# Performance work log

Hardware: AMD Instinct MI355X
Metric: run time of the kernel (lower is better)

## Reference

```python
import jax, jax.numpy as jnp
import numpy as np
from jax import lax

GRID_SIZE = 3


def setup_inputs() -> dict:
    key = jax.random.key(0)
    k1, k2, k3 = jax.random.split(key, 3)
    B, Cin, Cout, H, W, KH, KW, G = 32, 64, 64, 64, 64, 3, 3, GRID_SIZE
    x = jax.random.normal(k1, (B, Cin, H, W), dtype=jnp.float32)
    scale_base = jax.random.normal(k2, (Cout, Cin, KH, KW), dtype=jnp.float32) * 0.1
    scale_spline = jnp.ones((Cout, Cin, KH, KW), dtype=jnp.float32)
    coeff = jax.random.normal(k3, (2, Cout, Cin, KH, KW, G), dtype=jnp.float32) * 0.02
    bias = jnp.zeros((Cout,), dtype=jnp.float32)
    return {"x": x, "scale_base": scale_base, "scale_spline": scale_spline, "coeff": coeff, "bias": bias}


def _conv(x, w, padding=1):
    return lax.conv_general_dilated(
        x, w, window_strides=(1, 1), padding=((padding, padding), (padding, padding)),
        dimension_numbers=("NCHW", "OIHW", "NCHW"))


def reference(x, scale_base, scale_spline, coeff, bias):
    B, Cin, H, W = x.shape
    Cout, _, KH, KW = scale_base.shape
    G = coeff.shape[-1]
    # Fourier feature expansion: cos(k*x), sin(k*x) for k = 1..G
    ks = jnp.arange(1, G + 1, dtype=x.dtype)
    xk = x[:, :, None] * ks[None, None, :, None, None]          # (B, Cin, G, H, W)
    feats = jnp.concatenate([jnp.cos(xk), jnp.sin(xk)], axis=2)  # (B, Cin, 2G, H, W)
    feats = feats.reshape(B, Cin * 2 * G, H, W)
    # Spline weights: coeff (2, Cout, Cin, KH, KW, G) scaled per-tap -> (Cout, Cin*2G, KH, KW)
    w = coeff * scale_spline[None, :, :, :, :, None]
    w = jnp.transpose(w, (1, 2, 0, 5, 3, 4)).reshape(Cout, Cin * 2 * G, KH, KW)
    # Base branch: SiLU(x) convolved with scale_base
    base = jax.nn.silu(x)
    out = _conv(base, scale_base) + _conv(feats, w)
    out = out + bias[None, :, None, None]
    return out
```

## Files before the change

kernel.cpp:

```cpp
#include <hip/hip_runtime.h>

typedef __attribute__((ext_vector_type(8))) short bf16x8;
typedef __attribute__((ext_vector_type(4))) float f32x4;

#define FROW   4224
#define FBUF   42240
#define BGRP   36864
#define LDS_TOT (2 * FBUF + 2 * BGRP)

static __device__ __forceinline__ unsigned short f2bf(float f) {
  union { float f; unsigned u; } v; v.f = f;
  unsigned r = v.u + 0x7fffu + ((v.u >> 16) & 1u);
  return (unsigned short)(r >> 16);
}

static __device__ __forceinline__ void gload16(const void* g, void* l) {
  __builtin_amdgcn_global_load_lds(
      (const __attribute__((address_space(1))) void*)g,
      (__attribute__((address_space(3))) void*)l, 16, 0, 0);
}

__global__ void pack_w_k(const float* __restrict__ sb, const float* __restrict__ ss,
                         const float* __restrict__ cf, unsigned short* __restrict__ wpk) {
  int idx = blockIdx.x * 256 + threadIdx.x;
  if (idx >= 126 * 64 * 32) return;
  int e = idx & 7;
  int q = (idx >> 3) & 3;
  int co = (idx >> 5) & 63;
  int rest = idx >> 11;
  int tap = rest % 9;
  int c2 = rest / 9;
  int c = c2 >> 1, half = c2 & 1;
  int ci = half * 32 + q * 8 + e;
  int kh = tap / 3, kw = tap % 3;
  int wi = ((co * 64 + ci) * 3 + kh) * 3 + kw;
  float v;
  if (c == 0) {
    v = sb[wi];
  } else {
    int s = (c - 1) / 3, g = (c - 1) % 3;
    v = cf[(s * 36864 + wi) * 3 + g] * ss[wi];
  }
  wpk[((c2 * 9 + tap) * 64 + co) * 32 + ((q ^ ((co >> 1) & 3)) << 3) + e] = f2bf(v);
}

__global__ void feats_k(const float* __restrict__ x, unsigned short* __restrict__ fg) {
  __shared__ __align__(16) unsigned short lds[64 * 456];
  const int b = blockIdx.x, h = blockIdx.y;
  const int tid = threadIdx.x;
  const int w = tid & 63, cig = tid >> 6;
  const int key = ((w + 1) >> 1) & 3;
  const int base = w * 456;
#pragma unroll
  for (int i = 0; i < 16; ++i) {
    int ci = cig * 16 + i;
    float v = x[(((size_t)b * 64 + ci) * 64 + h) * 64 + w];
    float sg = 1.0f / (1.0f + __expf(-v));
    float f0 = v * sg;
    float s1, c1;
    __sincosf(v, &s1, &c1);
    float c2v = c1 * c1 - s1 * s1, s2v = 2.0f * s1 * c1;
    float c3v = c1 * c2v - s1 * s2v, s3v = s1 * c2v + c1 * s2v;
    int q = ci >> 3;
    int half = q >> 2, qq = q & 3;
    int sl = (half * 4 + (qq ^ key)) * 8 + (ci & 7);
    lds[base + 0 * 64 + sl] = f2bf(f0);
    lds[base + 1 * 64 + sl] = f2bf(c1);
    lds[base + 2 * 64 + sl] = f2bf(c2v);
    lds[base + 3 * 64 + sl] = f2bf(c3v);
    lds[base + 4 * 64 + sl] = f2bf(s1);
    lds[base + 5 * 64 + sl] = f2bf(s2v);
    lds[base + 6 * 64 + sl] = f2bf(s3v);
  }
  __syncthreads();
#pragma unroll
  for (int k = 0; k < 14; ++k) {
    int u = tid + k * 256;
    int qs = u & 3;
    int ww = (u >> 2) & 63;
    int c2i = u >> 8;
    int cc = c2i >> 1, half = c2i & 1;
    uint4 v = *(const uint4*)&lds[ww * 456 + cc * 64 + (half * 4 + qs) * 8];
    unsigned short* dst = fg + ((size_t)(c2i * 32 + b) * 64 + h) * 2048 + (ww * 4 + qs) * 8;
    *(uint4*)dst = v;
  }
}

__global__ __launch_bounds__(512, 2) void gemm_k(
    const unsigned short* __restrict__ fg, const unsigned short* __restrict__ wpk,
    const float* __restrict__ bias, float* __restrict__ out) {
  extern __shared__ __align__(16) char smem[];
  const int b = blockIdx.x;
  const int h0 = blockIdx.y * 8;
  const int tid = threadIdx.x;
  const int lane = tid & 63;
  const int wid = tid >> 6;
  const int l15 = lane & 15;
  const int lg = lane >> 4;
  const char* fgB = (const char*)fg;
  const char* wpkB = (const char*)wpk;

  for (int i = tid; i < 2 * FBUF / 4; i += 512) {
    int off = i * 4;
    int off2 = (off >= FBUF) ? off - FBUF : off;
    int row = off2 / FROW;
    int cb = off2 - row * FROW;
    int hh = h0 - 1 + row;
    bool staged = ((unsigned)hh < 64u) && (cb >= 64) && (cb < 4160);
    if (!staged) ((int*)smem)[i] = 0;
  }

#define STAGE_GRP(cn, fdst, bdst)                                                \
  for (int u = wid; u < 76; u += 8) {                                            \
    if (u < 40) {                                                                \
      int row = u >> 2, j = u & 3;                                               \
      int hh = h0 - 1 + row;                                                     \
      if ((unsigned)hh < 64u)                                                    \
        gload16(fgB + ((size_t)((cn) * 2048 + b * 64 + hh)) * 4096 +             \
                    j * 1024 + lane * 16,                                        \
                (fdst) + row * FROW + 64 + j * 1024);                            \
    } else {                                                                     \
      int t = u - 40;                                                            \
      int tap = t >> 2, part = t & 3;                                            \
      gload16(wpkB + (size_t)((cn) * 9 + tap) * 4096 + part * 1024 + lane * 16,  \
              (bdst) + tap * 4096 + part * 1024);                                \
    }                                                                            \
  }

  STAGE_GRP(0, smem, smem + 2 * FBUF);
  __syncthreads();

  f32x4 acc[4][4];
#pragma unroll
  for (int mf = 0; mf < 4; ++mf)
#pragma unroll
    for (int nf = 0; nf < 4; ++nf)
#pragma unroll
      for (int qq = 0; qq < 4; ++qq) acc[mf][nf][qq] = 0.0f;

  for (int c2 = 0; c2 < 14; ++c2) {
    const int cur = c2 & 1;
    char* f = smem + (cur ? FBUF : 0);
    char* bgc = smem + 2 * FBUF + (cur ? BGRP : 0);
    if (c2 < 13) {
      char* fnext = smem + (cur ? 0 : FBUF);
      char* bnext = smem + 2 * FBUF + (cur ? 0 : BGRP);
      STAGE_GRP(c2 + 1, fnext, bnext);
    }
#pragma unroll
    for (int tap = 0; tap < 9; ++tap) {
      const int kh = tap / 3, kw = tap - kh * 3;
      const int lrow = wid + kh;
      const char* bb = bgc + tap * 4096;

      bf16x8 A[4], Bv[4];
#pragma unroll
      for (int mf = 0; mf < 4; ++mf) {
        int col = mf * 16 + l15 + kw;
        A[mf] = *(const bf16x8*)(f + (lrow * 66 + col) * 64 + ((lg ^ ((col >> 1) & 3)) << 4));
      }
#pragma unroll
      for (int nf = 0; nf < 4; ++nf) {
        int co = nf * 16 + l15;
        Bv[nf] = *(const bf16x8*)(bb + co * 64 + ((lg ^ ((co >> 1) & 3)) << 4));
      }
#pragma unroll
      for (int mf = 0; mf < 4; ++mf)
#pragma unroll
        for (int nf = 0; nf < 4; ++nf)
          acc[mf][nf] = __builtin_amdgcn_mfma_f32_16x16x32_bf16(
              A[mf], Bv[nf], acc[mf][nf], 0, 0, 0);
    }
    __syncthreads();
  }
#undef STAGE_GRP

  const int h = h0 + wid;
#pragma unroll
  for (int mf = 0; mf < 4; ++mf) {
    int w4 = mf * 16 + (lg << 2);
#pragma unroll
    for (int nf = 0; nf < 4; ++nf) {
      int co = nf * 16 + l15;
      float bv = bias[co];
      f32x4 v = acc[mf][nf];
      f32x4 res;
      res[0] = v[0] + bv; res[1] = v[1] + bv; res[2] = v[2] + bv; res[3] = v[3] + bv;
      *(f32x4*)(out + ((size_t)(b * 64 + co) * 64 + h) * 64 + w4) = res;
    }
  }
}

__global__ void naive_k(const float* __restrict__ x, const float* __restrict__ sb,
                        const float* __restrict__ ss, const float* __restrict__ cf,
                        const float* __restrict__ bias, float* __restrict__ out) {
  int idx = blockIdx.x * 256 + threadIdx.x;
  if (idx >= 32 * 64 * 64 * 64) return;
  int w = idx & 63, h = (idx >> 6) & 63, co = (idx >> 12) & 63, b = idx >> 18;
  float acc = bias[co];
  for (int ci = 0; ci < 64; ++ci) {
    for (int kh = 0; kh < 3; ++kh) {
      int hh = h + kh - 1;
      if ((unsigned)hh >= 64u) continue;
      for (int kw = 0; kw < 3; ++kw) {
        int ww = w + kw - 1;
        if ((unsigned)ww >= 64u) continue;
        float v = x[((b * 64 + ci) * 64 + hh) * 64 + ww];
        int wi = ((co * 64 + ci) * 3 + kh) * 3 + kw;
        float s1, c1; __sincosf(v, &s1, &c1);
        float c2 = c1 * c1 - s1 * s1, s2 = 2.f * s1 * c1;
        float c3 = c1 * c2 - s1 * s2, s3 = s1 * c2 + c1 * s2;
        float t = sb[wi] * (v / (1.f + __expf(-v)));
        t += ss[wi] * (cf[wi * 3] * c1 + cf[wi * 3 + 1] * c2 + cf[wi * 3 + 2] * c3 +
                       cf[(36864 + wi) * 3] * s1 + cf[(36864 + wi) * 3 + 1] * s2 +
                       cf[(36864 + wi) * 3 + 2] * s3);
        acc += t;
      }
    }
  }
  out[idx] = acc;
}

extern "C" void kernel_launch(void* const* d_in, const int* in_sizes, int n_in,
                              void* d_out, int out_size, void* d_ws, size_t ws_size,
                              hipStream_t stream) {
  const float* x = (const float*)d_in[0];
  const float* sb = (const float*)d_in[1];
  const float* ss = (const float*)d_in[2];
  const float* cf = (const float*)d_in[3];
  const float* bias = (const float*)d_in[4];
  float* out = (float*)d_out;

  const size_t FEATS_OFF = 1u << 20;
  const size_t NEED = FEATS_OFF + (size_t)14 * 32 * 64 * 4096;
  if (ws_size >= NEED) {
    unsigned short* wpk = (unsigned short*)d_ws;
    unsigned short* fg = (unsigned short*)((char*)d_ws + FEATS_OFF);
    pack_w_k<<<1008, 256, 0, stream>>>(sb, ss, cf, wpk);
    feats_k<<<dim3(32, 64), 256, 0, stream>>>(x, fg);
    (void)hipFuncSetAttribute((const void*)gemm_k,
                              hipFuncAttributeMaxDynamicSharedMemorySize, LDS_TOT);
    gemm_k<<<dim3(32, 8), 512, LDS_TOT, stream>>>(fg, wpk, bias, out);
  } else {
    naive_k<<<32768, 256, 0, stream>>>(x, sb, ss, cf, bias, out);
  }
}
```

Measured before the change: 98.19 us.

## Split conv taps across two warp groups with 2-row tiles and LDS reduction

Each warp now computes two output rows instead of one. The 9 taps are split between two groups of 4 warps (taps 0-4 and 5-8), so each B-fragment load feeds twice as many MFMAs. The two groups' partial sums are reduced through swizzled LDS before the bias is added and the result stored. Per-lane LDS offsets are also hoisted out of the loop. In exchange the accumulator doubles to 128 floats per lane, which raises register pressure and may hurt the 2-blocks-per-CU target. The 5-vs-4 tap split is uneven, and the reduction adds an extra barrier.

Result: no change. 97.51 us (-0.7%).

```diff
diff --git a/kernel.cpp b/kernel.cpp
--- a/kernel.cpp
+++ b/kernel.cpp
@@ -97,6 +97,8 @@
   const int wid = tid >> 6;
   const int l15 = lane & 15;
   const int lg = lane >> 4;
+  const int grp = wid >> 2;
+  const int rowb = (wid & 3) * 2;
   const char* fgB = (const char*)fg;
   const char* wpkB = (const char*)wpk;
 
@@ -108,6 +110,18 @@
     int hh = h0 - 1 + row;
     bool staged = ((unsigned)hh < 64u) && (cb >= 64) && (cb < 4160);
     if (!staged) ((int*)smem)[i] = 0;
+  }
+
+  int aoff[4][3], boff[4];
+#pragma unroll
+  for (int cf = 0; cf < 4; ++cf) {
+#pragma unroll
+    for (int kw = 0; kw < 3; ++kw) {
+      int col = cf * 16 + l15 + kw;
+      aoff[cf][kw] = col * 64 + ((lg ^ ((col >> 1) & 3)) << 4);
+    }
+    int co = cf * 16 + l15;
+    boff[cf] = co * 64 + ((lg ^ ((co >> 1) & 3)) << 4);
   }
 
 #define STAGE_GRP(cn, fdst, bdst)                                                \
@@ -130,63 +144,96 @@
   STAGE_GRP(0, smem, smem + 2 * FBUF);
   __syncthreads();
 
-  f32x4 acc[4][4];
-#pragma unroll
-  for (int mf = 0; mf < 4; ++mf)
-#pragma unroll
-    for (int nf = 0; nf < 4; ++nf)
-#pragma unroll
-      for (int qq = 0; qq < 4; ++qq) acc[mf][nf][qq] = 0.0f;
+  f32x4 acc[2][4][4];
+#pragma unroll
+  for (int ro = 0; ro < 2; ++ro)
+#pragma unroll
+    for (int cfi = 0; cfi < 4; ++cfi)
+#pragma unroll
+      for (int nf = 0; nf < 4; ++nf)
+#pragma unroll
+        for (int qq = 0; qq < 4; ++qq) acc[ro][cfi][nf][qq] = 0.0f;
+
+#define COMP_TAP(T)                                                              \
+  {                                                                              \
+    const int kh_ = (T) / 3, kw_ = (T) % 3;                                      \
+    bf16x8 A[2][4], Bv[4];                                                       \
+    _Pragma("unroll")                                                            \
+    for (int ro = 0; ro < 2; ++ro) {                                             \
+      const char* rp = f + (rowb + ro + kh_) * FROW;                             \
+      _Pragma("unroll")                                                          \
+      for (int cfi = 0; cfi < 4; ++cfi)                                          \
+        A[ro][cfi] = *(const bf16x8*)(rp + aoff[cfi][kw_]);                      \
+    }                                                                            \
+    _Pragma("unroll")                                                            \
+    for (int nf = 0; nf < 4; ++nf)                                               \
+      Bv[nf] = *(const bf16x8*)(bgc + (T) * 4096 + boff[nf]);                    \
+    _Pragma("unroll")                                                            \
+    for (int ro = 0; ro < 2; ++ro)                                               \
+      _Pragma("unroll")                                                          \
+      for (int cfi = 0; cfi < 4; ++cfi)                                          \
+        _Pragma("unroll")                                                        \
+        for (int nf = 0; nf < 4; ++nf)                                           \
+          acc[ro][cfi][nf] = __builtin_amdgcn_mfma_f32_16x16x32_bf16(            \
+              A[ro][cfi], Bv[nf], acc[ro][cfi][nf], 0, 0, 0);                    \
+  }
 
   for (int c2 = 0; c2 < 14; ++c2) {
     const int cur = c2 & 1;
-    char* f = smem + (cur ? FBUF : 0);
-    char* bgc = smem + 2 * FBUF + (cur ? BGRP : 0);
+    const char* f = smem + (cur ? FBUF : 0);
+    const char* bgc = smem + 2 * FBUF + (cur ? BGRP : 0);
     if (c2 < 13) {
       char* fnext = smem + (cur ? 0 : FBUF);
       char* bnext = smem + 2 * FBUF + (cur ? 0 : BGRP);
       STAGE_GRP(c2 + 1, fnext, bnext);
     }
-#pragma unroll
-    for (int tap = 0; tap < 9; ++tap) {
-      const int kh = tap / 3, kw = tap - kh * 3;
-      const int lrow = wid + kh;
-      const char* bb = bgc + tap * 4096;
-
-      bf16x8 A[4], Bv[4];
-#pragma unroll
-      for (int mf = 0; mf < 4; ++mf) {
-        int col = mf * 16 + l15 + kw;
-        A[mf] = *(const bf16x8*)(f + (lrow * 66 + col) * 64 + ((lg ^ ((col >> 1) & 3)) << 4));
+    if (grp == 0) {
+      COMP_TAP(0) COMP_TAP(1) COMP_TAP(2) COMP_TAP(3) COMP_TAP(4)
+    } else {
+      COMP_TAP(5) COMP_TAP(6) COMP_TAP(7) COMP_TAP(8)
+    }
+    __syncthreads();
+  }
+#undef COMP_TAP
+#undef STAGE_GRP
+
+  if (grp == 1) {
+#pragma unroll
+    for (int ro = 0; ro < 2; ++ro)
+#pragma unroll
+      for (int cfi = 0; cfi < 4; ++cfi)
+#pragma unroll
+        for (int nf = 0; nf < 4; ++nf) {
+          int co = nf * 16 + l15;
+          int pxl = (rowb + ro) * 64 + cfi * 16 + (lg << 2);
+          float* p = (float*)smem + co * 512 + (pxl ^ ((co & 7) << 2));
+          *(f32x4*)p = acc[ro][cfi][nf];
+        }
+  }
+  __syncthreads();
+  if (grp == 0) {
+#pragma unroll
+    for (int ro = 0; ro < 2; ++ro) {
+      const int h = h0 + rowb + ro;
+#pragma unroll
+      for (int cfi = 0; cfi < 4; ++cfi) {
+        int w4 = cfi * 16 + (lg << 2);
+#pragma unroll
+        for (int nf = 0; nf < 4; ++nf) {
+          int co = nf * 16 + l15;
+          int pxl = (rowb + ro) * 64 + cfi * 16 + (lg << 2);
+          const float* p = (const float*)smem + co * 512 + (pxl ^ ((co & 7) << 2));
+          f32x4 part = *(const f32x4*)p;
+          float bv = bias[co];
+          f32x4 v = acc[ro][cfi][nf];
+          f32x4 res;
+          res[0] = v[0] + part[0] + bv;
+          res[1] = v[1] + part[1] + bv;
+          res[2] = v[2] + part[2] + bv;
+          res[3] = v[3] + part[3] + bv;
+          *(f32x4*)(out + ((size_t)(b * 64 + co) * 64 + h) * 64 + w4) = res;
+        }
       }
-#pragma unroll
-      for (int nf = 0; nf < 4; ++nf) {
-        int co = nf * 16 + l15;
-        Bv[nf] = *(const bf16x8*)(bb + co * 64 + ((lg ^ ((co >> 1) & 3)) << 4));
-      }
-#pragma unroll
-      for (int mf = 0; mf < 4; ++mf)
-#pragma unroll
-        for (int nf = 0; nf < 4; ++nf)
-          acc[mf][nf] = __builtin_amdgcn_mfma_f32_16x16x32_bf16(
-              A[mf], Bv[nf], acc[mf][nf], 0, 0, 0);
-    }
-    __syncthreads();
-  }
-#undef STAGE_GRP
-
-  const int h = h0 + wid;
-#pragma unroll
-  for (int mf = 0; mf < 4; ++mf) {
-    int w4 = mf * 16 + (lg << 2);
-#pragma unroll
-    for (int nf = 0; nf < 4; ++nf) {
-      int co = nf * 16 + l15;
-      float bv = bias[co];
-      f32x4 v = acc[mf][nf];
-      f32x4 res;
-      res[0] = v[0] + bv; res[1] = v[1] + bv; res[2] = v[2] + bv; res[3] = v[3] + bv;
-      *(f32x4*)(out + ((size_t)(b * 64 + co) * 64 + h) * 64 + w4) = res;
     }
   }
 }
```

## Fuse weight packing into feats kernel and pipeline GEMM per kernel row

Applied to the files above, without the earlier changes.

The weight-packing kernel is merged into the feature kernel, with each block packing 126 weight elements, which removes one launch. The GEMM block drops from 8 waves/8 rows to 4 waves/4 rows, so there are twice as many blocks and less LDS per block. B tiles are now double-buffered per kernel row (three taps) and features are staged in three chunks interleaved with compute, with precomputed LDS offsets. The extra barriers per channel group (three instead of one) and the smaller per-block reuse of B loads may offset the gains in occupancy and overlap.

After: 92.11 us. 6.2% less time.

```diff
diff --git a/kernel.cpp b/kernel.cpp
--- a/kernel.cpp
+++ b/kernel.cpp
@@ -4,9 +4,9 @@
 typedef __attribute__((ext_vector_type(4))) float f32x4;
 
 #define FROW   4224
-#define FBUF   42240
-#define BGRP   36864
-#define LDS_TOT (2 * FBUF + 2 * BGRP)
+#define FBUF4  25344
+#define BTRIO  12288
+#define LDS_T2 (2 * FBUF4 + 2 * BTRIO)
 
 static __device__ __forceinline__ unsigned short f2bf(float f) {
   union { float f; unsigned u; } v; v.f = f;
@@ -20,31 +20,9 @@
       (__attribute__((address_space(3))) void*)l, 16, 0, 0);
 }
 
-__global__ void pack_w_k(const float* __restrict__ sb, const float* __restrict__ ss,
-                         const float* __restrict__ cf, unsigned short* __restrict__ wpk) {
-  int idx = blockIdx.x * 256 + threadIdx.x;
-  if (idx >= 126 * 64 * 32) return;
-  int e = idx & 7;
-  int q = (idx >> 3) & 3;
-  int co = (idx >> 5) & 63;
-  int rest = idx >> 11;
-  int tap = rest % 9;
-  int c2 = rest / 9;
-  int c = c2 >> 1, half = c2 & 1;
-  int ci = half * 32 + q * 8 + e;
-  int kh = tap / 3, kw = tap % 3;
-  int wi = ((co * 64 + ci) * 3 + kh) * 3 + kw;
-  float v;
-  if (c == 0) {
-    v = sb[wi];
-  } else {
-    int s = (c - 1) / 3, g = (c - 1) % 3;
-    v = cf[(s * 36864 + wi) * 3 + g] * ss[wi];
-  }
-  wpk[((c2 * 9 + tap) * 64 + co) * 32 + ((q ^ ((co >> 1) & 3)) << 3) + e] = f2bf(v);
-}
-
-__global__ void feats_k(const float* __restrict__ x, unsigned short* __restrict__ fg) {
+__global__ void feats_k(const float* __restrict__ x, const float* __restrict__ sb,
+                        const float* __restrict__ ss, const float* __restrict__ cf,
+                        unsigned short* __restrict__ fg, unsigned short* __restrict__ wpk) {
   __shared__ __align__(16) unsigned short lds[64 * 456];
   const int b = blockIdx.x, h = blockIdx.y;
   const int tid = threadIdx.x;
@@ -84,14 +62,35 @@
     unsigned short* dst = fg + ((size_t)(c2i * 32 + b) * 64 + h) * 2048 + (ww * 4 + qs) * 8;
     *(uint4*)dst = v;
   }
-}
-
-__global__ __launch_bounds__(512, 2) void gemm_k(
+  if (tid < 126) {
+    int idx = (b * 64 + h) * 126 + tid;
+    int e = idx & 7;
+    int q = (idx >> 3) & 3;
+    int co = (idx >> 5) & 63;
+    int rest = idx >> 11;
+    int tap = rest % 9;
+    int c2p = rest / 9;
+    int c = c2p >> 1, half = c2p & 1;
+    int ci = half * 32 + q * 8 + e;
+    int kh = tap / 3, kw = tap % 3;
+    int wi = ((co * 64 + ci) * 3 + kh) * 3 + kw;
+    float v;
+    if (c == 0) {
+      v = sb[wi];
+    } else {
+      int s = (c - 1) / 3, g = (c - 1) % 3;
+      v = cf[(s * 36864 + wi) * 3 + g] * ss[wi];
+    }
+    wpk[((c2p * 9 + tap) * 64 + co) * 32 + ((q ^ ((co >> 1) & 3)) << 3) + e] = f2bf(v);
+  }
+}
+
+__global__ __launch_bounds__(256, 2) void gemm_k(
     const unsigned short* __restrict__ fg, const unsigned short* __restrict__ wpk,
     const float* __restrict__ bias, float* __restrict__ out) {
   extern __shared__ __align__(16) char smem[];
   const int b = blockIdx.x;
-  const int h0 = blockIdx.y * 8;
+  const int h0 = blockIdx.y * 4;
   const int tid = threadIdx.x;
   const int lane = tid & 63;
   const int wid = tid >> 6;
@@ -100,9 +99,9 @@
   const char* fgB = (const char*)fg;
   const char* wpkB = (const char*)wpk;
 
-  for (int i = tid; i < 2 * FBUF / 4; i += 512) {
+  for (int i = tid; i < 2 * FBUF4 / 4; i += 256) {
     int off = i * 4;
-    int off2 = (off >= FBUF) ? off - FBUF : off;
+    int off2 = (off >= FBUF4) ? off - FBUF4 : off;
     int row = off2 / FROW;
     int cb = off2 - row * FROW;
     int hh = h0 - 1 + row;
@@ -110,80 +109,97 @@
     if (!staged) ((int*)smem)[i] = 0;
   }
 
-#define STAGE_GRP(cn, fdst, bdst)                                                \
-  for (int u = wid; u < 76; u += 8) {                                            \
-    if (u < 40) {                                                                \
-      int row = u >> 2, j = u & 3;                                               \
-      int hh = h0 - 1 + row;                                                     \
-      if ((unsigned)hh < 64u)                                                    \
-        gload16(fgB + ((size_t)((cn) * 2048 + b * 64 + hh)) * 4096 +             \
-                    j * 1024 + lane * 16,                                        \
-                (fdst) + row * FROW + 64 + j * 1024);                            \
-    } else {                                                                     \
-      int t = u - 40;                                                            \
-      int tap = t >> 2, part = t & 3;                                            \
-      gload16(wpkB + (size_t)((cn) * 9 + tap) * 4096 + part * 1024 + lane * 16,  \
-              (bdst) + tap * 4096 + part * 1024);                                \
-    }                                                                            \
-  }
-
-  STAGE_GRP(0, smem, smem + 2 * FBUF);
+  int aoff[4][3], boff[4];
+#pragma unroll
+  for (int cf = 0; cf < 4; ++cf) {
+#pragma unroll
+    for (int kw = 0; kw < 3; ++kw) {
+      int col = cf * 16 + l15 + kw;
+      aoff[cf][kw] = col * 64 + ((lg ^ ((col >> 1) & 3)) << 4);
+    }
+    int co = cf * 16 + l15;
+    boff[cf] = co * 64 + ((lg ^ ((co >> 1) & 3)) << 4);
+  }
+
+#define STAGE_TRIO(cn, khn, bdst)                                                \
+  _Pragma("unroll")                                                              \
+  for (int i = 0; i < 3; ++i) {                                                  \
+    int u = i * 4 + wid;                        \
+    gload16(wpkB + (size_t)((cn) * 9 + (khn) * 3 + (u >> 2)) * 4096 +            \
+                (u & 3) * 1024 + lane * 16,                                      \
+            (bdst) + (u >> 2) * 4096 + (u & 3) * 1024);                          \
+  }
+#define STAGE_F8(cn, khp, fdst)                                                  \
+  _Pragma("unroll")                                                              \
+  for (int j = 0; j < 2; ++j) {                                                  \
+    int k = (khp) * 8 + wid * 2 + j;                                  \
+    int row = k >> 2, part = k & 3;                                              \
+    int hh = h0 - 1 + row;                                                       \
+    if ((unsigned)hh < 64u)                                                      \
+      gload16(fgB + ((size_t)((cn) * 2048 + b * 64 + hh)) * 4096 +               \
+                  part * 1024 + lane * 16,                                       \
+              (fdst) + row * FROW + 64 + part * 1024);                           \
+  }
+
+#pragma unroll
+  for (int p = 0; p < 3; ++p) { STAGE_F8(0, p, smem) }
+  STAGE_TRIO(0, 0, smem + 2 * FBUF4)
   __syncthreads();
 
   f32x4 acc[4][4];
 #pragma unroll
-  for (int mf = 0; mf < 4; ++mf)
+  for (int cfi = 0; cfi < 4; ++cfi)
 #pragma unroll
     for (int nf = 0; nf < 4; ++nf)
 #pragma unroll
-      for (int qq = 0; qq < 4; ++qq) acc[mf][nf][qq] = 0.0f;
+      for (int qq = 0; qq < 4; ++qq) acc[cfi][nf][qq] = 0.0f;
 
   for (int c2 = 0; c2 < 14; ++c2) {
-    const int cur = c2 & 1;
-    char* f = smem + (cur ? FBUF : 0);
-    char* bgc = smem + 2 * FBUF + (cur ? BGRP : 0);
-    if (c2 < 13) {
-      char* fnext = smem + (cur ? 0 : FBUF);
-      char* bnext = smem + 2 * FBUF + (cur ? 0 : BGRP);
-      STAGE_GRP(c2 + 1, fnext, bnext);
-    }
-#pragma unroll
-    for (int tap = 0; tap < 9; ++tap) {
-      const int kh = tap / 3, kw = tap - kh * 3;
-      const int lrow = wid + kh;
-      const char* bb = bgc + tap * 4096;
-
-      bf16x8 A[4], Bv[4];
-#pragma unroll
-      for (int mf = 0; mf < 4; ++mf) {
-        int col = mf * 16 + l15 + kw;
-        A[mf] = *(const bf16x8*)(f + (lrow * 66 + col) * 64 + ((lg ^ ((col >> 1) & 3)) << 4));
+    const char* f = smem + ((c2 & 1) ? FBUF4 : 0);
+    char* fnext = smem + (((c2 + 1) & 1) ? FBUF4 : 0);
+#pragma unroll
+    for (int kh = 0; kh < 3; ++kh) {
+      const int khg = c2 * 3 + kh;
+      const char* bb = smem + 2 * FBUF4 + ((khg & 1) ? BTRIO : 0);
+      if (khg < 41) {
+        char* bnext = smem + 2 * FBUF4 + (((khg + 1) & 1) ? BTRIO : 0);
+        const int cn = (khg + 1) / 3, khn = (khg + 1) % 3;
+        STAGE_TRIO(cn, khn, bnext)
       }
-#pragma unroll
-      for (int nf = 0; nf < 4; ++nf) {
-        int co = nf * 16 + l15;
-        Bv[nf] = *(const bf16x8*)(bb + co * 64 + ((lg ^ ((co >> 1) & 3)) << 4));
+      if (c2 < 13) { STAGE_F8(c2 + 1, kh, fnext) }
+
+      const char* frow = f + (wid + kh) * FROW;
+#pragma unroll
+      for (int kw = 0; kw < 3; ++kw) {
+        bf16x8 A[4], Bv[4];
+#pragma unroll
+        for (int cfi = 0; cfi < 4; ++cfi)
+          A[cfi] = *(const bf16x8*)(frow + aoff[cfi][kw]);
+#pragma unroll
+        for (int nf = 0; nf < 4; ++nf)
+          Bv[nf] = *(const bf16x8*)(bb + kw * 4096 + boff[nf]);
+#pragma unroll
+        for (int cfi = 0; cfi < 4; ++cfi)
+#pragma unroll
+          for (int nf = 0; nf < 4; ++nf)
+            acc[cfi][nf] = __builtin_amdgcn_mfma_f32_16x16x32_bf16(
+                A[cfi], Bv[nf], acc[cfi][nf], 0, 0, 0);
       }
-#pragma unroll
-      for (int mf = 0; mf < 4; ++mf)
-#pragma unroll
-        for (int nf = 0; nf < 4; ++nf)
-          acc[mf][nf] = __builtin_amdgcn_mfma_f32_16x16x32_bf16(
-              A[mf], Bv[nf], acc[mf][nf], 0, 0, 0);
-    }
-    __syncthreads();
-  }
-#undef STAGE_GRP
+      __syncthreads();
+    }
+  }
+#undef STAGE_TRIO
+#undef STAGE_F8
 
   const int h = h0 + wid;
 #pragma unroll
-  for (int mf = 0; mf < 4; ++mf) {
-    int w4 = mf * 16 + (lg << 2);
+  for (int cfi = 0; cfi < 4; ++cfi) {
+    int w4 = cfi * 16 + (lg << 2);
 #pragma unroll
     for (int nf = 0; nf < 4; ++nf) {
       int co = nf * 16 + l15;
       float bv = bias[co];
-      f32x4 v = acc[mf][nf];
+      f32x4 v = acc[cfi][nf];
       f32x4 res;
       res[0] = v[0] + bv; res[1] = v[1] + bv; res[2] = v[2] + bv; res[3] = v[3] + bv;
       *(f32x4*)(out + ((size_t)(b * 64 + co) * 64 + h) * 64 + w4) = res;
@@ -236,11 +252,10 @@
   if (ws_size >= NEED) {
     unsigned short* wpk = (unsigned short*)d_ws;
     unsigned short* fg = (unsigned short*)((char*)d_ws + FEATS_OFF);
-    pack_w_k<<<1008, 256, 0, stream>>>(sb, ss, cf, wpk);
-    feats_k<<<dim3(32, 64), 256, 0, stream>>>(x, fg);
+    feats_k<<<dim3(32, 64), 256, 0, stream>>>(x, sb, ss, cf, fg, wpk);
     (void)hipFuncSetAttribute((const void*)gemm_k,
-                              hipFuncAttributeMaxDynamicSharedMemorySize, LDS_TOT);
-    gemm_k<<<dim3(32, 8), 512, LDS_TOT, stream>>>(fg, wpk, bias, out);
+                              hipFuncAttributeMaxDynamicSharedMemorySize, LDS_T2);
+    gemm_k<<<dim3(32, 16), 256, LDS_T2, stream>>>(fg, wpk, bias, out);
   } else {
     naive_k<<<32768, 256, 0, stream>>>(x, sb, ss, cf, bias, out);
   }
```
